# Kernel optimization log

Hardware: AMD Instinct MI355X
Metric: run time of the kernel (lower is better)

The kernel has to match this reference:

```python
import jax, jax.numpy as jnp
import numpy as np

N, C, H, W = 16, 512, 64, 64
C_BAR, C_HAT = 64, 256


def max_pool2(t):
    # t: [n, c, h, w] -> [n, c, h//2, w//2] via 2x2 max pool
    n, c, h, w = t.shape
    return t.reshape(n, c, h // 2, 2, w // 2, 2).max(axis=(3, 5))


def setup_inputs() -> dict:
    key = jax.random.key(0)
    ks = jax.random.split(key, 6)
    x = jax.random.normal(ks[0], (N, C, H, W), dtype=jnp.float32)
    # 1x1 conv weights stored as [out_channels, in_channels]
    w_theta = jax.random.normal(ks[1], (C_BAR, C), dtype=jnp.float32) * 0.02
    w_phi = jax.random.normal(ks[2], (C_BAR, C), dtype=jnp.float32) * 0.02
    w_g = jax.random.normal(ks[3], (C_HAT, C), dtype=jnp.float32) * 0.02
    w_o = jax.random.normal(ks[4], (C, C_HAT), dtype=jnp.float32) * 0.02
    # gamma initialized to zero in the module; use a small nonzero value so the
    # attention path contributes to the output (and to gradients).
    gamma = jnp.full((1,), 0.1, dtype=jnp.float32)
    return {"x": x, "w_theta": w_theta, "w_phi": w_phi, "w_g": w_g,
            "w_o": w_o, "gamma": gamma}


def reference(x, w_theta, w_phi, w_g, w_o, gamma):
    n, c, h, w = x.shape
    hw, hw4 = h * w, (h * w) // 4
    # 1x1 conv projections (pure channel GEMMs)
    g_x = jnp.einsum('nchw,oc->nohw', x, w_g)          # [n, c_hat, h, w]
    g_x = max_pool2(g_x).reshape(n, -1, hw4)            # [n, c_hat, hw/4]
    phi_x = jnp.einsum('nchw,oc->nohw', x, w_phi)       # [n, c_bar, h, w]
    phi_x = max_pool2(phi_x).reshape(n, -1, hw4)        # [n, c_bar, hw/4]
    theta_x = jnp.einsum('nchw,oc->nohw', x, w_theta).reshape(n, -1, hw)  # [n, c_bar, hw]
    # bmm -> softmax -> bmm
    scores = jnp.einsum('nds,ndt->nst', theta_x, phi_x)  # [n, hw, hw/4]
    attn = jax.nn.softmax(scores, axis=-1)
    y = jnp.einsum('ndt,nst->nds', g_x, attn)            # [n, c_hat, hw]
    y = y.reshape(n, -1, h, w)
    o = jnp.einsum('nchw,oc->nohw', y, w_o)              # [n, c, h, w]
    return gamma[0] * o + x
```

## Files before the change

kernel.cpp:

```cpp
#include <hip/hip_runtime.h>
#include <stdint.h>

typedef unsigned short u16;
typedef u16   us4 __attribute__((ext_vector_type(4)));
typedef u16   us8 __attribute__((ext_vector_type(8)));
typedef __bf16 bf8 __attribute__((ext_vector_type(8)));
typedef float f4  __attribute__((ext_vector_type(4)));

__device__ __forceinline__ u16 f2bf(float f) {
    uint32_t u = __builtin_bit_cast(uint32_t, f);
    uint32_t r = (u + 0x7fffu + ((u >> 16) & 1u)) >> 16;
    return (u16)r;
}
__device__ __forceinline__ float bf2f(u16 s) {
    uint32_t u = ((uint32_t)s) << 16;
    return __builtin_bit_cast(float, u);
}
__device__ __forceinline__ f4 mfma16(bf8 a, bf8 b, f4 c) {
    return __builtin_amdgcn_mfma_f32_16x16x32_bf16(a, b, c, 0, 0, 0);
}
__device__ __forceinline__ u16 max4bf(u16 a, u16 b, u16 c, u16 d) {
    float m = fmaxf(fmaxf(bf2f(a), bf2f(b)), fmaxf(bf2f(c), bf2f(d)));
    return f2bf(m);
}

__global__ __launch_bounds__(256) void xt_kernel(
    const float* __restrict__ x, u16* __restrict__ Xt)
{
    const int s0 = blockIdx.x * 64, c0 = blockIdx.y * 64, n = blockIdx.z;
    const int tid = threadIdx.x;
    __shared__ u16 lds[64 * 72];

    {
        int c_loc = tid & 63, s_seg = (tid >> 6) * 16;
        const float* src = x + ((size_t)n * 512 + c0 + c_loc) * 4096 + s0 + s_seg;
        for (int i4 = 0; i4 < 4; i4++) {
            float4 f = *(const float4*)(src + i4 * 4);
            int s = s_seg + i4 * 4;
            lds[(s + 0) * 72 + c_loc] = f2bf(f.x);
            lds[(s + 1) * 72 + c_loc] = f2bf(f.y);
            lds[(s + 2) * 72 + c_loc] = f2bf(f.z);
            lds[(s + 3) * 72 + c_loc] = f2bf(f.w);
        }
    }
    __syncthreads();
    {
        int s_loc = tid >> 2, c_seg = (tid & 3) * 16;
        u16* dst = Xt + ((size_t)n * 4096 + s0 + s_loc) * 512 + c0 + c_seg;
        *(us8*)(dst)     = *(const us8*)&lds[s_loc * 72 + c_seg];
        *(us8*)(dst + 8) = *(const us8*)&lds[s_loc * 72 + c_seg + 8];
    }
}

__global__ __launch_bounds__(256) void wconv_kernel(
    const float* __restrict__ w_theta, const float* __restrict__ w_phi,
    const float* __restrict__ w_g, const float* __restrict__ w_o,
    u16* __restrict__ Wall_bf, u16* __restrict__ Wo_bf)
{
    int base = (blockIdx.x * 256 + threadIdx.x) * 4;
    const float* src; u16* dst;
    if (base < 32768)       { src = w_theta + base;          dst = Wall_bf + base; }
    else if (base < 65536)  { src = w_phi + (base - 32768);  dst = Wall_bf + base; }
    else if (base < 196608) { src = w_g + (base - 65536);    dst = Wall_bf + base; }
    else                    { src = w_o + (base - 196608);   dst = Wo_bf + (base - 196608); }
    float4 f = *(const float4*)src;
    us4 v; v[0] = f2bf(f.x); v[1] = f2bf(f.y); v[2] = f2bf(f.z); v[3] = f2bf(f.w);
    *(us4*)dst = v;
}

__global__ __launch_bounds__(256) void projT_gemm(
    const u16* __restrict__ Xt, const u16* __restrict__ Wall_bf,
    u16* __restrict__ PT)
{
    const int s0 = blockIdx.x * 128;
    const int r0 = blockIdx.y * 128;
    const int nb = blockIdx.z;
    const int tid = threadIdx.x;
    const int wave = tid >> 6, lane = tid & 63;
    const int quad = lane >> 4, l15 = lane & 15;
    const int wm = (wave >> 1) * 64, wn = (wave & 1) * 64;

    __shared__ u16 a_lds[128 * 40];
    __shared__ u16 b_lds[128 * 40];

    f4 acc[4][4];
    f4 z = {0.f, 0.f, 0.f, 0.f};
    for (int i = 0; i < 4; i++) for (int j = 0; j < 4; j++) acc[i][j] = z;

    const u16* Abase = Xt + ((size_t)nb * 4096 + s0) * 512;
    const int m = tid >> 1, kseg = (tid & 1) * 16;

    for (int k0 = 0; k0 < 512; k0 += 32) {
        *(us8*)&a_lds[m * 40 + kseg]     = *(const us8*)(Abase + (size_t)m * 512 + k0 + kseg);
        *(us8*)&a_lds[m * 40 + kseg + 8] = *(const us8*)(Abase + (size_t)m * 512 + k0 + kseg + 8);
        *(us8*)&b_lds[m * 40 + kseg]     = *(const us8*)(Wall_bf + (size_t)(r0 + m) * 512 + k0 + kseg);
        *(us8*)&b_lds[m * 40 + kseg + 8] = *(const us8*)(Wall_bf + (size_t)(r0 + m) * 512 + k0 + kseg + 8);
        __syncthreads();
        bf8 af[4], bfr[4];
        for (int i = 0; i < 4; i++)
            af[i]  = __builtin_bit_cast(bf8, *(const us8*)&a_lds[(wm + i*16 + l15)*40 + quad*8]);
        for (int j = 0; j < 4; j++)
            bfr[j] = __builtin_bit_cast(bf8, *(const us8*)&b_lds[(wn + j*16 + l15)*40 + quad*8]);
        for (int i = 0; i < 4; i++)
            for (int j = 0; j < 4; j++)
                acc[i][j] = mfma16(af[i], bfr[j], acc[i][j]);
        __syncthreads();
    }
    for (int i = 0; i < 4; i++) {
        int s_idx = s0 + wm + i * 16 + quad * 4;
        for (int rr = 0; rr < 4; rr++) {
            u16* dst = PT + ((size_t)nb * 4096 + s_idx + rr) * 384 + r0 + wn + l15;
            for (int j = 0; j < 4; j++)
                dst[j * 16] = f2bf(acc[i][j][rr]);
        }
    }
}

__global__ __launch_bounds__(256) void phi_pool2(
    const u16* __restrict__ PT, u16* __restrict__ phiT)
{
    int n = blockIdx.y, t0 = blockIdx.x * 64;
    int tid = threadIdx.x;
    int t_loc = tid >> 2, d0 = (tid & 3) * 16;
    int t = t0 + t_loc;
    int h2 = t >> 5, w2 = t & 31;
    int s00 = h2 * 128 + w2 * 2;
    const u16* base = PT + ((size_t)n * 4096) * 384 + 64 + d0;
    us8 r[4][2];
    int soff[4] = {s00, s00 + 1, s00 + 64, s00 + 65};
    for (int p = 0; p < 4; p++) {
        r[p][0] = *(const us8*)(base + (size_t)soff[p] * 384);
        r[p][1] = *(const us8*)(base + (size_t)soff[p] * 384 + 8);
    }
    us8 o0, o1;
    for (int i = 0; i < 8; i++) {
        o0[i] = max4bf(r[0][0][i], r[1][0][i], r[2][0][i], r[3][0][i]);
        o1[i] = max4bf(r[0][1][i], r[1][1][i], r[2][1][i], r[3][1][i]);
    }
    u16* dst = phiT + ((size_t)n * 1024 + t) * 64 + d0;
    *(us8*)dst = o0;
    *(us8*)(dst + 8) = o1;
}

__global__ __launch_bounds__(256) void g_poolT(
    const u16* __restrict__ PT, u16* __restrict__ gP)
{
    int t0 = blockIdx.x * 64, d0 = blockIdx.y * 64, n = blockIdx.z;
    int tid = threadIdx.x;
    __shared__ u16 lds[64 * 72];

    {
        int t_loc = tid & 63, dseg = (tid >> 6) * 16;
        int t = t0 + t_loc;
        int h2 = t >> 5, w2 = t & 31;
        int s00 = h2 * 128 + w2 * 2;
        const u16* base = PT + ((size_t)n * 4096) * 384 + 128 + d0 + dseg;
        us8 r[4][2];
        int soff[4] = {s00, s00 + 1, s00 + 64, s00 + 65};
        for (int p = 0; p < 4; p++) {
            r[p][0] = *(const us8*)(base + (size_t)soff[p] * 384);
            r[p][1] = *(const us8*)(base + (size_t)soff[p] * 384 + 8);
        }
        for (int i = 0; i < 8; i++) {
            lds[(dseg + i) * 72 + t_loc]     = max4bf(r[0][0][i], r[1][0][i], r[2][0][i], r[3][0][i]);
            lds[(dseg + 8 + i) * 72 + t_loc] = max4bf(r[0][1][i], r[1][1][i], r[2][1][i], r[3][1][i]);
        }
    }
    __syncthreads();
    {
        int d_loc = tid >> 2, t_seg = (tid & 3) * 16;
        u16* dst = gP + ((size_t)n * 256 + d0 + d_loc) * 1024 + t0 + t_seg;
        *(us8*)(dst)     = *(const us8*)&lds[d_loc * 72 + t_seg];
        *(us8*)(dst + 8) = *(const us8*)&lds[d_loc * 72 + t_seg + 8];
    }
}

__global__ __launch_bounds__(256) void attn_kernel(
    const u16* __restrict__ PT, const u16* __restrict__ phiT,
    const u16* __restrict__ gP, u16* __restrict__ yT)
{
    int n = blockIdx.y;
    int tid = threadIdx.x;
    int wave = tid >> 6, lane = tid & 63, quad = lane >> 4, l15 = lane & 15;
    int q0 = blockIdx.x * 64 + wave * 16;

    __shared__ u16 phi_lds[32 * 72];
    __shared__ u16 g_lds[256 * 40];
    __shared__ u16 p_lds[4][16 * 40];

    const u16* th = PT + ((size_t)n * 4096 + q0 + l15) * 384 + quad * 8;
    bf8 bth0 = __builtin_bit_cast(bf8, *(const us8*)(th));
    bf8 bth1 = __builtin_bit_cast(bf8, *(const us8*)(th + 32));

    const int t_loc = tid >> 3, d0 = (tid & 7) * 8;
    const u16* phi_src = phiT + ((size_t)n * 1024 + t_loc) * 64 + d0;
    const u16* g_src   = gP + ((size_t)n * 256 + tid) * 1024;

    f4 z = {0.f, 0.f, 0.f, 0.f};
    f4 acc[16];
    for (int b = 0; b < 16; b++) acc[b] = z;
    float lsum = 0.f;

    us8 pf_phi = *(const us8*)(phi_src);
    us8 pf_g0  = *(const us8*)(g_src + 0);
    us8 pf_g1  = *(const us8*)(g_src + 8);
    us8 pf_g2  = *(const us8*)(g_src + 16);
    us8 pf_g3  = *(const us8*)(g_src + 24);
    *(us8*)&phi_lds[t_loc * 72 + d0] = pf_phi;
    *(us8*)&g_lds[tid * 40 + 0]  = pf_g0;
    *(us8*)&g_lds[tid * 40 + 8]  = pf_g1;
    *(us8*)&g_lds[tid * 40 + 16] = pf_g2;
    *(us8*)&g_lds[tid * 40 + 24] = pf_g3;
    __syncthreads();

    for (int ci = 0; ci < 32; ci++) {
        int nc = (ci + 1 < 32) ? (ci + 1) : ci;
        pf_phi = *(const us8*)(phi_src + (size_t)nc * 2048);
        pf_g0  = *(const us8*)(g_src + nc * 32 + 0);
        pf_g1  = *(const us8*)(g_src + nc * 32 + 8);
        pf_g2  = *(const us8*)(g_src + nc * 32 + 16);
        pf_g3  = *(const us8*)(g_src + nc * 32 + 24);

        for (int tt = 0; tt < 32; tt += 16) {
            bf8 ap0 = __builtin_bit_cast(bf8, *(const us8*)&phi_lds[(tt + l15) * 72 + quad * 8]);
            bf8 ap1 = __builtin_bit_cast(bf8, *(const us8*)&phi_lds[(tt + l15) * 72 + 32 + quad * 8]);
            f4 s = mfma16(ap0, bth0, z);
            s = mfma16(ap1, bth1, s);
            us4 pk;
            float ps = 0.f;
            for (int rr = 0; rr < 4; rr++) {
                float p = __expf(s[rr]);
                ps += p;
                pk[rr] = f2bf(p);
            }
            lsum += ps;
            *(us4*)&p_lds[wave][l15 * 40 + tt + quad * 4] = pk;
        }
        bf8 bp = __builtin_bit_cast(bf8, *(const us8*)&p_lds[wave][l15 * 40 + quad * 8]);
        for (int b = 0; b < 16; b++) {
            bf8 ag = __builtin_bit_cast(bf8, *(const us8*)&g_lds[(b * 16 + l15) * 40 + quad * 8]);
            acc[b] = mfma16(ag, bp, acc[b]);
        }
        __syncthreads();
        *(us8*)&phi_lds[t_loc * 72 + d0] = pf_phi;
        *(us8*)&g_lds[tid * 40 + 0]  = pf_g0;
        *(us8*)&g_lds[tid * 40 + 8]  = pf_g1;
        *(us8*)&g_lds[tid * 40 + 16] = pf_g2;
        *(us8*)&g_lds[tid * 40 + 24] = pf_g3;
        __syncthreads();
    }

    float v = lsum;
    v += __shfl_xor(v, 16);
    v += __shfl_xor(v, 32);
    float inv = 1.0f / v;

    u16* dst = yT + ((size_t)n * 4096 + q0 + l15) * 256 + quad * 4;
    for (int b = 0; b < 16; b++) {
        us4 o;
        for (int rr = 0; rr < 4; rr++) o[rr] = f2bf(acc[b][rr] * inv);
        *(us4*)(dst + b * 16) = o;
    }
}

__global__ __launch_bounds__(256) void oproj_gemm(
    const u16* __restrict__ Wo_bf, const u16* __restrict__ yT,
    const float* __restrict__ x, const float* __restrict__ gamma,
    float* __restrict__ out)
{
    const int nt = blockIdx.x;
    const int mt = blockIdx.y;
    const int nb = blockIdx.z;
    const int tid = threadIdx.x;
    const int wave = tid >> 6, lane = tid & 63;
    const int quad = lane >> 4, l15 = lane & 15;
    const int wm = (wave >> 1) * 32, wn = (wave & 1) * 64;
    const int s0 = nt * 128;

    __shared__ u16 a_lds[64 * 40];
    __shared__ u16 b_lds[128 * 40];

    f4 acc[2][4];
    f4 z = {0.f, 0.f, 0.f, 0.f};
    for (int i = 0; i < 2; i++) for (int j = 0; j < 4; j++) acc[i][j] = z;

    for (int k0 = 0; k0 < 256; k0 += 32) {
        {
            int m = tid >> 2, kq = (tid & 3) * 8;
            *(us8*)&a_lds[m * 40 + kq] =
                *(const us8*)(Wo_bf + (size_t)(mt * 64 + m) * 256 + k0 + kq);
        }
        {
            int s_loc = tid >> 1, kq = (tid & 1) * 16;
            const u16* src = yT + ((size_t)nb * 4096 + s0 + s_loc) * 256 + k0 + kq;
            *(us8*)&b_lds[s_loc * 40 + kq]     = *(const us8*)(src);
            *(us8*)&b_lds[s_loc * 40 + kq + 8] = *(const us8*)(src + 8);
        }
        __syncthreads();
        bf8 af[2], bfr[4];
        for (int i = 0; i < 2; i++)
            af[i] = __builtin_bit_cast(bf8, *(const us8*)&a_lds[(wm + i*16 + l15)*40 + quad*8]);
        for (int j = 0; j < 4; j++)
            bfr[j] = __builtin_bit_cast(bf8, *(const us8*)&b_lds[(wn + j*16 + l15)*40 + quad*8]);
        for (int i = 0; i < 2; i++)
            for (int j = 0; j < 4; j++)
                acc[i][j] = mfma16(af[i], bfr[j], acc[i][j]);
        __syncthreads();
    }
    float g0 = gamma[0];
    for (int i = 0; i < 2; i++) {
        int c = mt * 64 + wm + i * 16 + quad * 4;
        for (int j = 0; j < 4; j++) {
            int s = s0 + wn + j * 16 + l15;
            for (int rr = 0; rr < 4; rr++) {
                size_t idx = ((size_t)nb * 512 + c + rr) * 4096 + s;
                out[idx] = g0 * acc[i][j][rr] + x[idx];
            }
        }
    }
}

extern "C" void kernel_launch(void* const* d_in, const int* in_sizes, int n_in,
                              void* d_out, int out_size, void* d_ws, size_t ws_size,
                              hipStream_t stream)
{
    (void)in_sizes; (void)n_in; (void)out_size; (void)ws_size;
    const float* x       = (const float*)d_in[0];
    const float* w_theta = (const float*)d_in[1];
    const float* w_phi   = (const float*)d_in[2];
    const float* w_g     = (const float*)d_in[3];
    const float* w_o     = (const float*)d_in[4];
    const float* gamma   = (const float*)d_in[5];
    float* out = (float*)d_out;

    char* ws = (char*)d_ws;
    u16* Xt      = (u16*)(ws);
    u16* yT      = (u16*)(ws);
    u16* phiT    = (u16*)(ws + 33554432);
    u16* gP      = (u16*)(ws + 35651584);
    u16* Wall_bf = (u16*)(ws + 67108864);
    u16* Wo_bf   = (u16*)(ws + 67502080);
    u16* PT      = (u16*)(ws + 67764224);

    xt_kernel  <<<dim3(64, 8, 16), 256, 0, stream>>>(x, Xt);
    wconv_kernel<<<320, 256, 0, stream>>>(w_theta, w_phi, w_g, w_o, Wall_bf, Wo_bf);
    projT_gemm <<<dim3(32, 3, 16), 256, 0, stream>>>(Xt, Wall_bf, PT);
    phi_pool2  <<<dim3(16, 16),    256, 0, stream>>>(PT, phiT);
    g_poolT    <<<dim3(16, 4, 16), 256, 0, stream>>>(PT, gP);
    attn_kernel<<<dim3(64, 16),    256, 0, stream>>>(PT, phiT, gP, yT);
    oproj_gemm <<<dim3(32, 8, 16), 256, 0, stream>>>(Wo_bf, yT, x, gamma, out);
}
```

Baseline: 433.8 us.

## Double query tile per wave in attention, double-buffer LDS, enlarge oproj tile

The attention kernel now handles 32 queries per wave (two 16-query fragments), so each g and phi tile loaded into LDS feeds twice as many MFMAs. Its LDS staging is double-buffered, which removes one barrier per chunk, and the g loads are rearranged for better coalescing. The output projection GEMM tile grows from 64x128 to 128x128 per block, so each yT tile is reused across more output channels. The costs are more accumulator registers and LDS per block, and half as many blocks in both kernels (512 attention blocks), which can reduce occupancy.

```diff
diff --git a/kernel.cpp b/kernel.cpp
--- a/kernel.cpp
+++ b/kernel.cpp
@@ -175,91 +175,94 @@
     }
 }
 
-__global__ __launch_bounds__(256) void attn_kernel(
+__global__ __launch_bounds__(256, 2) void attn_kernel(
     const u16* __restrict__ PT, const u16* __restrict__ phiT,
     const u16* __restrict__ gP, u16* __restrict__ yT)
 {
     int n = blockIdx.y;
     int tid = threadIdx.x;
     int wave = tid >> 6, lane = tid & 63, quad = lane >> 4, l15 = lane & 15;
-    int q0 = blockIdx.x * 64 + wave * 16;
-
-    __shared__ u16 phi_lds[32 * 72];
-    __shared__ u16 g_lds[256 * 40];
-    __shared__ u16 p_lds[4][16 * 40];
-
-    const u16* th = PT + ((size_t)n * 4096 + q0 + l15) * 384 + quad * 8;
-    bf8 bth0 = __builtin_bit_cast(bf8, *(const us8*)(th));
-    bf8 bth1 = __builtin_bit_cast(bf8, *(const us8*)(th + 32));
+    int q0w = blockIdx.x * 128 + wave * 32;
+
+    __shared__ u16 phi_buf[2][32 * 72];
+    __shared__ u16 g_buf[2][256 * 40];
+    __shared__ u16 p_lds[4][2][16 * 40];
+
+    bf8 bth[2][2];
+    for (int j = 0; j < 2; j++) {
+        const u16* th = PT + ((size_t)n * 4096 + q0w + j * 16 + l15) * 384 + quad * 8;
+        bth[j][0] = __builtin_bit_cast(bf8, *(const us8*)(th));
+        bth[j][1] = __builtin_bit_cast(bf8, *(const us8*)(th + 32));
+    }
 
     const int t_loc = tid >> 3, d0 = (tid & 7) * 8;
     const u16* phi_src = phiT + ((size_t)n * 1024 + t_loc) * 64 + d0;
-    const u16* g_src   = gP + ((size_t)n * 256 + tid) * 1024;
+    const int gr = tid >> 2, gt = (tid & 3) * 8;
+    const u16* g_src = gP + ((size_t)n * 256 + gr) * 1024 + gt;
 
     f4 z = {0.f, 0.f, 0.f, 0.f};
-    f4 acc[16];
-    for (int b = 0; b < 16; b++) acc[b] = z;
-    float lsum = 0.f;
-
-    us8 pf_phi = *(const us8*)(phi_src);
-    us8 pf_g0  = *(const us8*)(g_src + 0);
-    us8 pf_g1  = *(const us8*)(g_src + 8);
-    us8 pf_g2  = *(const us8*)(g_src + 16);
-    us8 pf_g3  = *(const us8*)(g_src + 24);
-    *(us8*)&phi_lds[t_loc * 72 + d0] = pf_phi;
-    *(us8*)&g_lds[tid * 40 + 0]  = pf_g0;
-    *(us8*)&g_lds[tid * 40 + 8]  = pf_g1;
-    *(us8*)&g_lds[tid * 40 + 16] = pf_g2;
-    *(us8*)&g_lds[tid * 40 + 24] = pf_g3;
+    f4 acc[16][2];
+    for (int b = 0; b < 16; b++) { acc[b][0] = z; acc[b][1] = z; }
+    float lsum[2] = {0.f, 0.f};
+
+    *(us8*)&phi_buf[0][t_loc * 72 + d0] = *(const us8*)(phi_src);
+    for (int p = 0; p < 4; p++)
+        *(us8*)&g_buf[0][(p * 64 + gr) * 40 + gt] =
+            *(const us8*)(g_src + (size_t)p * 64 * 1024);
     __syncthreads();
 
     for (int ci = 0; ci < 32; ci++) {
+        int cur = ci & 1, nxt = cur ^ 1;
         int nc = (ci + 1 < 32) ? (ci + 1) : ci;
-        pf_phi = *(const us8*)(phi_src + (size_t)nc * 2048);
-        pf_g0  = *(const us8*)(g_src + nc * 32 + 0);
-        pf_g1  = *(const us8*)(g_src + nc * 32 + 8);
-        pf_g2  = *(const us8*)(g_src + nc * 32 + 16);
-        pf_g3  = *(const us8*)(g_src + nc * 32 + 24);
+        us8 pf_phi = *(const us8*)(phi_src + (size_t)nc * 2048);
+        us8 pf_g[4];
+        for (int p = 0; p < 4; p++)
+            pf_g[p] = *(const us8*)(g_src + (size_t)p * 64 * 1024 + nc * 32);
 
         for (int tt = 0; tt < 32; tt += 16) {
-            bf8 ap0 = __builtin_bit_cast(bf8, *(const us8*)&phi_lds[(tt + l15) * 72 + quad * 8]);
-            bf8 ap1 = __builtin_bit_cast(bf8, *(const us8*)&phi_lds[(tt + l15) * 72 + 32 + quad * 8]);
-            f4 s = mfma16(ap0, bth0, z);
-            s = mfma16(ap1, bth1, s);
-            us4 pk;
-            float ps = 0.f;
-            for (int rr = 0; rr < 4; rr++) {
-                float p = __expf(s[rr]);
-                ps += p;
-                pk[rr] = f2bf(p);
+            bf8 ap0 = __builtin_bit_cast(bf8, *(const us8*)&phi_buf[cur][(tt + l15) * 72 + quad * 8]);
+            bf8 ap1 = __builtin_bit_cast(bf8, *(const us8*)&phi_buf[cur][(tt + l15) * 72 + 32 + quad * 8]);
+            for (int j = 0; j < 2; j++) {
+                f4 s = mfma16(ap0, bth[j][0], z);
+                s = mfma16(ap1, bth[j][1], s);
+                us4 pk;
+                float ps = 0.f;
+                for (int rr = 0; rr < 4; rr++) {
+                    float p = __expf(s[rr]);
+                    ps += p;
+                    pk[rr] = f2bf(p);
+                }
+                lsum[j] += ps;
+                *(us4*)&p_lds[wave][j][l15 * 40 + tt + quad * 4] = pk;
             }
-            lsum += ps;
-            *(us4*)&p_lds[wave][l15 * 40 + tt + quad * 4] = pk;
-        }
-        bf8 bp = __builtin_bit_cast(bf8, *(const us8*)&p_lds[wave][l15 * 40 + quad * 8]);
+        }
+        bf8 bp0 = __builtin_bit_cast(bf8, *(const us8*)&p_lds[wave][0][l15 * 40 + quad * 8]);
+        bf8 bp1 = __builtin_bit_cast(bf8, *(const us8*)&p_lds[wave][1][l15 * 40 + quad * 8]);
         for (int b = 0; b < 16; b++) {
-            bf8 ag = __builtin_bit_cast(bf8, *(const us8*)&g_lds[(b * 16 + l15) * 40 + quad * 8]);
-            acc[b] = mfma16(ag, bp, acc[b]);
-        }
-        __syncthreads();
-        *(us8*)&phi_lds[t_loc * 72 + d0] = pf_phi;
-        *(us8*)&g_lds[tid * 40 + 0]  = pf_g0;
-        *(us8*)&g_lds[tid * 40 + 8]  = pf_g1;
-        *(us8*)&g_lds[tid * 40 + 16] = pf_g2;
-        *(us8*)&g_lds[tid * 40 + 24] = pf_g3;
-        __syncthreads();
-    }
-
-    float v = lsum;
-    v += __shfl_xor(v, 16);
-    v += __shfl_xor(v, 32);
-    float inv = 1.0f / v;
-
-    u16* dst = yT + ((size_t)n * 4096 + q0 + l15) * 256 + quad * 4;
-    for (int b = 0; b < 16; b++) {
-        us4 o;
-        for (int rr = 0; rr < 4; rr++) o[rr] = f2bf(acc[b][rr] * inv);
-        *(us4*)(dst + b * 16) = o;
+            bf8 ag = __builtin_bit_cast(bf8, *(const us8*)&g_buf[cur][(b * 16 + l15) * 40 + quad * 8]);
+            acc[b][0] = mfma16(ag, bp0, acc[b][0]);
+            acc[b][1] = mfma16(ag, bp1, acc[b][1]);
+        }
+        *(us8*)&phi_buf[nxt][t_loc * 72 + d0] = pf_phi;
+        for (int p = 0; p < 4; p++)
+            *(us8*)&g_buf[nxt][(p * 64 + gr) * 40 + gt] = pf_g[p];
+        __syncthreads();
+    }
+
+    float inv[2];
+    for (int j = 0; j < 2; j++) {
+        float v = lsum[j];
+        v += __shfl_xor(v, 16);
+        v += __shfl_xor(v, 32);
+        inv[j] = 1.0f / v;
+    }
+    for (int j = 0; j < 2; j++) {
+        u16* dst = yT + ((size_t)n * 4096 + q0w + j * 16 + l15) * 256 + quad * 4;
+        for (int b = 0; b < 16; b++) {
+            us4 o;
+            for (int rr = 0; rr < 4; rr++) o[rr] = f2bf(acc[b][j][rr] * inv[j]);
+            *(us4*)(dst + b * 16) = o;
+        }
     }
 }
 
@@ -268,48 +271,43 @@
     const float* __restrict__ x, const float* __restrict__ gamma,
     float* __restrict__ out)
 {
-    const int nt = blockIdx.x;
-    const int mt = blockIdx.y;
+    const int s0 = blockIdx.x * 128;
+    const int c0 = blockIdx.y * 128;
     const int nb = blockIdx.z;
     const int tid = threadIdx.x;
     const int wave = tid >> 6, lane = tid & 63;
     const int quad = lane >> 4, l15 = lane & 15;
-    const int wm = (wave >> 1) * 32, wn = (wave & 1) * 64;
-    const int s0 = nt * 128;
-
-    __shared__ u16 a_lds[64 * 40];
+    const int wm = (wave >> 1) * 64, wn = (wave & 1) * 64;
+
+    __shared__ u16 a_lds[128 * 40];
     __shared__ u16 b_lds[128 * 40];
 
-    f4 acc[2][4];
+    f4 acc[4][4];
     f4 z = {0.f, 0.f, 0.f, 0.f};
-    for (int i = 0; i < 2; i++) for (int j = 0; j < 4; j++) acc[i][j] = z;
+    for (int i = 0; i < 4; i++) for (int j = 0; j < 4; j++) acc[i][j] = z;
+
+    const int m = tid >> 1, kseg = (tid & 1) * 16;
+    const u16* Bbase = yT + ((size_t)nb * 4096 + s0) * 256;
 
     for (int k0 = 0; k0 < 256; k0 += 32) {
-        {
-            int m = tid >> 2, kq = (tid & 3) * 8;
-            *(us8*)&a_lds[m * 40 + kq] =
-                *(const us8*)(Wo_bf + (size_t)(mt * 64 + m) * 256 + k0 + kq);
-        }
-        {
-            int s_loc = tid >> 1, kq = (tid & 1) * 16;
-            const u16* src = yT + ((size_t)nb * 4096 + s0 + s_loc) * 256 + k0 + kq;
-            *(us8*)&b_lds[s_loc * 40 + kq]     = *(const us8*)(src);
-            *(us8*)&b_lds[s_loc * 40 + kq + 8] = *(const us8*)(src + 8);
-        }
-        __syncthreads();
-        bf8 af[2], bfr[4];
-        for (int i = 0; i < 2; i++)
-            af[i] = __builtin_bit_cast(bf8, *(const us8*)&a_lds[(wm + i*16 + l15)*40 + quad*8]);
+        *(us8*)&a_lds[m * 40 + kseg]     = *(const us8*)(Wo_bf + (size_t)(c0 + m) * 256 + k0 + kseg);
+        *(us8*)&a_lds[m * 40 + kseg + 8] = *(const us8*)(Wo_bf + (size_t)(c0 + m) * 256 + k0 + kseg + 8);
+        *(us8*)&b_lds[m * 40 + kseg]     = *(const us8*)(Bbase + (size_t)m * 256 + k0 + kseg);
+        *(us8*)&b_lds[m * 40 + kseg + 8] = *(const us8*)(Bbase + (size_t)m * 256 + k0 + kseg + 8);
+        __syncthreads();
+        bf8 af[4], bfr[4];
+        for (int i = 0; i < 4; i++)
+            af[i]  = __builtin_bit_cast(bf8, *(const us8*)&a_lds[(wm + i*16 + l15)*40 + quad*8]);
         for (int j = 0; j < 4; j++)
             bfr[j] = __builtin_bit_cast(bf8, *(const us8*)&b_lds[(wn + j*16 + l15)*40 + quad*8]);
-        for (int i = 0; i < 2; i++)
+        for (int i = 0; i < 4; i++)
             for (int j = 0; j < 4; j++)
                 acc[i][j] = mfma16(af[i], bfr[j], acc[i][j]);
         __syncthreads();
     }
     float g0 = gamma[0];
-    for (int i = 0; i < 2; i++) {
-        int c = mt * 64 + wm + i * 16 + quad * 4;
+    for (int i = 0; i < 4; i++) {
+        int c = c0 + wm + i * 16 + quad * 4;
         for (int j = 0; j < 4; j++) {
             int s = s0 + wn + j * 16 + l15;
             for (int rr = 0; rr < 4; rr++) {
@@ -347,6 +345,6 @@
     projT_gemm <<<dim3(32, 3, 16), 256, 0, stream>>>(Xt, Wall_bf, PT);
     phi_pool2  <<<dim3(16, 16),    256, 0, stream>>>(PT, phiT);
     g_poolT    <<<dim3(16, 4, 16), 256, 0, stream>>>(PT, gP);
-    attn_kernel<<<dim3(64, 16),    256, 0, stream>>>(PT, phiT, gP, yT);
-    oproj_gemm <<<dim3(32, 8, 16), 256, 0, stream>>>(Wo_bf, yT, x, gamma, out);
-}
+    attn_kernel<<<dim3(32, 16),    256, 0, stream>>>(PT, phiT, gP, yT);
+    oproj_gemm <<<dim3(32, 4, 16), 256, 0, stream>>>(Wo_bf, yT, x, gamma, out);
+}
```

Measured after the change: 500.4 us. 1.15x slower.
